# Performance work log

Hardware: AMD Instinct MI355X
Metric: run time of the kernel (lower is better)

The kernel has to match this reference:

```python
import jax, jax.numpy as jnp
import numpy as np

N = 100000; E = 1600000; G = 2000; S = 40; MAXP = 50
IN = 64; F = 128; H = 4; HD = F // H; FFN = 8 * F
EPS = 1e-5; BN_EPS = 1e-5

def _ln(x, g, b):
    m = jnp.mean(x, -1, keepdims=True)
    v = jnp.mean((x - m) ** 2, -1, keepdims=True)
    return (x - m) * jax.lax.rsqrt(v + EPS) * g + b

def setup_inputs():
    key = jax.random.key(0)
    ks = jax.random.split(key, 16)
    def lin(k, i, o):
        kw, kb = jax.random.split(k)
        lim = 1.0 / np.sqrt(i)
        return (jax.random.uniform(kw, (i, o), jnp.float32, -lim, lim),
                jax.random.uniform(kb, (o,), jnp.float32, -lim, lim))
    W_gcn, b_gcn = lin(ks[1], IN, F)
    Wq, bq = lin(ks[2], F, F); Wk, bk = lin(ks[3], F, F)
    Wv, bv = lin(ks[4], F, F); Wo, bo = lin(ks[5], F, F)
    W1, b1 = lin(ks[6], F, FFN); W2, b2 = lin(ks[7], FFN, F)
    Wg, bg = lin(ks[8], 2 * F, F)
    ones = lambda: jnp.ones((F,), jnp.float32)
    zeros = lambda: jnp.zeros((F,), jnp.float32)
    return {
        'x': jax.random.normal(ks[0], (N, IN), jnp.float32),
        'edge_index': jax.random.randint(ks[9], (2, E), 0, N),
        'batch': jnp.repeat(jnp.arange(G), N // G),
        'set_batch': jnp.repeat(jnp.arange(S), G // S),
        'W_gcn': W_gcn, 'b_gcn': b_gcn,
        'bn_g': ones(), 'bn_b': zeros(),
        'lnpre_g': ones(), 'lnpre_b': zeros(),
        'Wq': Wq, 'bq': bq, 'Wk': Wk, 'bk': bk, 'Wv': Wv, 'bv': bv, 'Wo': Wo, 'bo': bo,
        'ln1_g': ones(), 'ln1_b': zeros(),
        'W1': W1, 'b1': b1, 'W2': W2, 'b2': b2,
        'ln2_g': ones(), 'ln2_b': zeros(),
        'Wg': Wg, 'bg': bg,
    }

def _forward(x, W_gcn, b_gcn, bn_g, bn_b, lnpre_g, lnpre_b, Wq, bq, Wk, bk, Wv, bv, Wo, bo, ln1_g, ln1_b, W1, b1, W2, b2, ln2_g, ln2_b, Wg, bg, edge_index, batch, set_batch):
    row, col = edge_index[0], edge_index[1]
    # GCNConv, improved=True -> self-loop weight 2.0 (PyG gcn_norm)
    xw = x @ W_gcn                                              # [N,F]
    deg = jax.ops.segment_sum(jnp.ones(E, xw.dtype), col, N) + 2.0
    dinv = jax.lax.rsqrt(deg)
    norm = dinv[row] * dinv[col]                                # [E]
    agg = jax.ops.segment_sum(xw[row] * norm[:, None], col, N)  # scatter-add to targets
    h = agg + (2.0 * dinv * dinv)[:, None] * xw + b_gcn
    # BatchNorm1d eval (running_mean=0, running_var=1) + ReLU; dropout is identity in eval
    h = jax.nn.relu(h * jax.lax.rsqrt(jnp.asarray(1.0 + BN_EPS, h.dtype)) * bn_g + bn_b)
    # global mean pool per graph
    cnt_g = jax.ops.segment_sum(jnp.ones(N, h.dtype), batch, G)
    z = jax.ops.segment_sum(h, batch, G) / cnt_g[:, None]       # [G,F]
    # to_dense_batch over sets (set_batch is sorted)
    cnt_s = jax.ops.segment_sum(jnp.ones(G, jnp.int32), set_batch, S)
    starts = jnp.cumsum(cnt_s) - cnt_s
    pos = jnp.arange(G) - starts[set_batch]                     # position within set
    zd = jnp.zeros((S, MAXP, F), z.dtype).at[set_batch, pos].set(z)
    mask = jnp.arange(MAXP)[None, :] < cnt_s[:, None]           # [S,MAXP]
    # pre-LN MHA with key_padding_mask
    zn = _ln(zd, lnpre_g, lnpre_b)
    q = (zn @ Wq + bq).reshape(S, MAXP, H, HD)
    k = (zn @ Wk + bk).reshape(S, MAXP, H, HD)
    v = (zn @ Wv + bv).reshape(S, MAXP, H, HD)
    scores = jnp.einsum('sqhd,skhd->shqk', q, k) / np.sqrt(HD)
    scores = jnp.where(mask[:, None, None, :], scores, -1e9)
    attn = jax.nn.softmax(scores, -1)
    o = jnp.einsum('shqk,skhd->sqhd', attn, v).reshape(S, MAXP, F) @ Wo + bo
    zd = _ln(zd + o, ln1_g, ln1_b)
    # FFN block (post-LN residual)
    f = jax.nn.relu(zd @ W1 + b1) @ W2 + b2
    zd = _ln(zd + f, ln2_g, ln2_b)
    # z_dense[mask] ordering == gather via (set_batch, pos); broadcast to nodes
    set_info = zd[set_batch, pos][batch]                        # [N,F]
    # gated fusion
    gate = jax.nn.sigmoid(jnp.concatenate([h, set_info], -1) @ Wg + bg)
    return gate * set_info + (1.0 - gate) * h

def reference(x, edge_index, batch, set_batch, W_gcn, b_gcn, bn_g, bn_b, lnpre_g, lnpre_b, Wq, bq, Wk, bk, Wv, bv, Wo, bo, ln1_g, ln1_b, W1, b1, W2, b2, ln2_g, ln2_b, Wg, bg):
    return _forward(x, W_gcn, b_gcn, bn_g, bn_b, lnpre_g, lnpre_b, Wq, bq, Wk, bk, Wv, bv, Wo, bo, ln1_g, ln1_b, W1, b1, W2, b2, ln2_g, ln2_b, Wg, bg, edge_index, batch, set_batch)
```

## Files before the change

kernel.cpp:

```cpp
#include <hip/hip_runtime.h>
#include <hip/hip_bf16.h>
#include <cstddef>

#define NN 100000
#define NE 1600000
#define NG 2000
#define NS 40
#define INF 64
#define F 128
#define FFN_DIM 1024
#define NB 782
#define BCAP 3072
#define SC_BLOCKS 512
#define SC_CHUNK 3125
#define KSPLIT 8

using bf16 = __hip_bfloat16;
typedef __attribute__((ext_vector_type(8))) short short8;
typedef __attribute__((ext_vector_type(4))) float f32x4;
typedef __attribute__((ext_vector_type(2))) float f32x2;

__device__ __forceinline__ short f2bs(float f){
    union { bf16 b; short s; } u; u.b = __float2bfloat16(f); return u.s;
}
__device__ __forceinline__ unsigned int pk2(float a, float b){
    return (unsigned int)(unsigned short)f2bs(a) | ((unsigned int)(unsigned short)f2bs(b) << 16);
}

__global__ __launch_bounds__(256) void k_initw(int* __restrict__ bcursor,
                                               const float* __restrict__ Wq, const float* __restrict__ Wk,
                                               const float* __restrict__ Wv, const float* __restrict__ W1,
                                               const float* __restrict__ W2, const float* __restrict__ Wg,
                                               unsigned short* __restrict__ Wqb, unsigned short* __restrict__ Wkb,
                                               unsigned short* __restrict__ Wvb, unsigned short* __restrict__ W1b,
                                               unsigned short* __restrict__ W2b, unsigned short* __restrict__ Wgb){
    int t = blockIdx.x*256 + threadIdx.x;
    int stride = gridDim.x*256;
    for (int i=t; i<NB; i+=stride) bcursor[i] = i*BCAP;
    for (int i=t; i<16384; i+=stride){
        int k = i>>7, n = i&127;
        Wqb[n*128+k] = (unsigned short)f2bs(Wq[(size_t)k*F+n]);
        Wkb[n*128+k] = (unsigned short)f2bs(Wk[(size_t)k*F+n]);
        Wvb[n*128+k] = (unsigned short)f2bs(Wv[(size_t)k*F+n]);
        Wgb[n*128+k] = (unsigned short)f2bs(Wg[(size_t)k*F+n]);
    }
    for (int i=t; i<131072; i+=stride){
        int k = i>>10, n = i&1023;
        W1b[(size_t)n*128+k] = (unsigned short)f2bs(W1[(size_t)k*FFN_DIM+n]);
    }
    for (int i=t; i<131072; i+=stride){
        int n = i>>10, k = i&1023;
        W2b[(size_t)n*1024+k] = (unsigned short)f2bs(W2[(size_t)k*F+n]);
    }
}

__global__ __launch_bounds__(256) void k_xws(const float* __restrict__ x, const float* __restrict__ W,
                                             const float* __restrict__ dinv, unsigned char* __restrict__ xws8){
    __shared__ short Xs[128*72];
    __shared__ short Ws[128*72];
    int t = threadIdx.x;
    int rowBase = blockIdx.x * 128;
    #pragma unroll
    for (int i=0;i<32;i++){
        int id = i*256+t; int k = id>>7, n = id&127;
        Ws[n*72 + k] = f2bs(W[id]);
    }
    #pragma unroll
    for (int i=0;i<8;i++){
        int id = i*256+t;
        int r = id>>4; int k4 = (id&15)*4;
        int row = rowBase + r; if (row >= NN) row = NN-1;
        float4 v = *(const float4*)&x[(size_t)row*INF + k4];
        *(unsigned int*)&Xs[r*72 + k4]     = pk2(v.x, v.y);
        *(unsigned int*)&Xs[r*72 + k4 + 2] = pk2(v.z, v.w);
    }
// ... 10 lines not shown
        int kb = ks*32 + quad*8;
        short8 b0 = *(const short8*)&Xs[((w  )*16 + lr)*72 + kb];
        short8 b1 = *(const short8*)&Xs[((w+4)*16 + lr)*72 + kb];
        #pragma unroll
        for (int mt=0; mt<8; ++mt){
            short8 a = *(const short8*)&Ws[(mt*16 + lr)*72 + kb];
            acc[0][mt] = __builtin_amdgcn_mfma_f32_16x16x32_bf16(a, b0, acc[0][mt], 0, 0, 0);
            acc[1][mt] = __builtin_amdgcn_mfma_f32_16x16x32_bf16(a, b1, acc[1][mt], 0, 0, 0);
        }
    }
    #pragma unroll
    for (int rt=0; rt<2; ++rt){
        int row = rowBase + (w + rt*4)*16 + lr;
        if (row < NN){
            float dv = dinv[row];
            #pragma unroll
            for (int mt=0; mt<8; ++mt){
                int p = __builtin_amdgcn_cvt_pk_fp8_f32(acc[rt][mt][0]*dv, acc[rt][mt][1]*dv, 0, false);
                p     = __builtin_amdgcn_cvt_pk_fp8_f32(acc[rt][mt][2]*dv, acc[rt][mt][3]*dv, p, true);
                *(int*)&xws8[(size_t)row*F + mt*16 + quad*4] = p;
            }
        }
    }
}

__global__ __launch_bounds__(1024) void k_scatter2(const int* __restrict__ ei, int* __restrict__ bcursor,
                                                   int* __restrict__ ebuf){
    __shared__ int lh[NB];
    __shared__ int lb[NB];
    int t = threadIdx.x;
    int base = blockIdx.x * SC_CHUNK;
    for (int b=t; b<NB; b+=1024) lh[b] = 0;
    __syncthreads();
    int rr[4], cc[4];
    #pragma unroll
    for (int q=0;q<4;q++){
        int i = t + q*1024;
        bool v = (i < SC_CHUNK);
        int idx = v ? (base + i) : base;
        rr[q] = ei[idx];
        cc[q] = ei[NE + idx];
        if (v) atomicAdd(&lh[cc[q]>>7], 1);
    }
    __syncthreads();
    for (int b=t; b<NB; b+=1024){
        int n = lh[b];
        lb[b] = n ? atomicAdd(&bcursor[b], n) : 0;
        lh[b] = 0;
    }
    __syncthreads();
    #pragma unroll
    for (int q=0;q<4;q++){
        int i = t + q*1024;
        if (i < SC_CHUNK){
            int b = cc[q] >> 7;
            int rk = atomicAdd(&lh[b], 1);
            ebuf[lb[b] + rk] = (rr[q] << 7) | (cc[q] & 127);
        }
    }
}

__global__ __launch_bounds__(256) void k_sort(const int* __restrict__ ebuf, const int* __restrict__ bcursor,
                                              int* __restrict__ cnt, float* __restrict__ dinv,
                                              int* __restrict__ nstart, int* __restrict__ ebuf2){
    __shared__ int lh[128];
    __shared__ int s[128];
    __shared__ int lcur[128];
    __shared__ int sorted[BCAP];
    int t = threadIdx.x;
    int b = blockIdx.x;
    int e0 = b * BCAP;
    int nE = bcursor[b] - e0;
    if (t < 128) lh[t] = 0;
    __syncthreads();
    for (int i=t; i<nE; i+=256) atomicAdd(&lh[ebuf[e0+i] & 127], 1);
    __syncthreads();
    int c = (t < 128) ? lh[t] : 0;
    if (t < 128) s[t] = c;
    __syncthreads();
    #pragma unroll
    for (int off=1; off<128; off<<=1){
        int v = (t >= off && t < 128) ? s[t-off] : 0;
        __syncthreads();
        if (t < 128) s[t] += v;
        __syncthreads();
    }
    int node = b*128 + t;
    if (t < 128){
        int excl = s[t] - c;
        lcur[t] = excl;
        if (node < NN){
            nstart[node] = e0 + excl;
            cnt[node] = c;
            dinv[node] = rsqrtf((float)c + 2.0f);
        }
    }
    __syncthreads();
    for (int i=t; i<nE; i+=256){
        int v = ebuf[e0 + i];
        int nl = v & 127;
        int rk = atomicAdd(&lcur[nl], 1);
        sorted[rk] = (v >> 7) << 5;
    }
    __syncthreads();
    for (int i=t; i<nE; i+=256) ebuf2[e0 + i] = sorted[i];
}

__global__ __launch_bounds__(256) void k_aggpool(const unsigned char* __restrict__ xws8,
                                                 const int* __restrict__ nstart, const int* __restrict__ cnt,
                                                 const float* __restrict__ dinv, const float* __restrict__ b_gcn,
                                                 const float* __restrict__ bn_g, const float* __restrict__ bn_b,
                                                 const int* __restrict__ ebuf2,
                                                 const float* __restrict__ lnpre_g, const float* __restrict__ lnpre_b,
                                                 float* __restrict__ h, unsigned short* __restrict__ hb,
                                                 float* __restrict__ z, unsigned short* __restrict__ znb){
    __shared__ float zacc[4][128];
    int t = threadIdx.x;
    int lane = t & 63, w = t >> 6;
    int half = lane >> 5, lh = lane & 31;
    int g = blockIdx.x;
    const unsigned int* xw32 = (const unsigned int*)xws8;
    unsigned int* hb32 = (unsigned int*)hb;
    unsigned int* znb32 = (unsigned int*)znb;

    float4 bg4  = *(const float4*)&b_gcn[4*lh];
    float4 bng4 = *(const float4*)&bn_g[4*lh];
    float4 bnb4 = *(const float4*)&bn_b[4*lh];
    const float bns = rsqrtf(1.f + 1e-5f);
// ... 75 lines not shown
        float s2 = ((v0.z+v1.z)+(v2.z+v3.z)) / 50.0f;
        float s3 = ((v0.w+v1.w)+(v2.w+v3.w)) / 50.0f;
        if (half == 0)
            *(float4*)&z[(size_t)g*F + 4*lh] = make_float4(s0,s1,s2,s3);
        float s = (s0+s1)+(s2+s3);
        #pragma unroll
        for (int off=1; off<32; off<<=1) s += __shfl_xor(s, off);
        float m = s * (1.f/128.f);
        float d0=s0-m, d1=s1-m, d2=s2-m, d3=s3-m;
        float vv = (d0*d0+d1*d1)+(d2*d2+d3*d3);
        #pragma unroll
        for (int off=1; off<32; off<<=1) vv += __shfl_xor(vv, off);
        float rs = rsqrtf(vv*(1.f/128.f) + 1e-5f);
        float4 lg = *(const float4*)&lnpre_g[4*lh];
        float4 lb = *(const float4*)&lnpre_b[4*lh];
        if (half == 0){
            float o0 = d0*rs*lg.x+lb.x, o1 = d1*rs*lg.y+lb.y;
            float o2 = d2*rs*lg.z+lb.z, o3 = d3*rs*lg.w+lb.w;
            *(uint2*)&znb32[(size_t)g*64 + 2*lh] = make_uint2(pk2(o0,o1), pk2(o2,o3));
        }
    }
}

__global__ __launch_bounds__(256) void k_qkv_g(const unsigned short* __restrict__ znb,
                                               const unsigned short* __restrict__ Wqb,
                                               const unsigned short* __restrict__ Wkb,
                                               const unsigned short* __restrict__ Wvb,
                                               const float* __restrict__ bq, const float* __restrict__ bk,
                                               const float* __restrict__ bv,
                                               float* __restrict__ Cq, float* __restrict__ Ck,
                                               float* __restrict__ Cv){
    int zsel = blockIdx.z;
    const unsigned short* B = (zsel==0)?Wqb:(zsel==1)?Wkb:Wvb;
    const float* bias = (zsel==0)?bq:(zsel==1)?bk:bv;
    float* C = (zsel==0)?Cq:(zsel==1)?Ck:Cv;
    int t = threadIdx.x;
    int lane = t & 63, w = t >> 6;
    int lr = lane & 15, quad = lane >> 4;
    int mrow0 = blockIdx.x*64 + w*16;
    f32x4 acc[8];
    #pragma unroll
    for (int j=0;j<8;j++) acc[j] = (f32x4){0.f,0.f,0.f,0.f};
    #pragma unroll
    for (int ks=0; ks<4; ++ks){
        int kb = ks*32 + quad*8;
        int row = mrow0 + lr;
        if (row >= NG) row = NG-1;
        short8 a = *(const short8*)&znb[(size_t)row*F + kb];
        #pragma unroll
        for (int nt=0; nt<8; ++nt){
            short8 b = *(const short8*)&B[(size_t)(nt*16 + lr)*128 + kb];
            acc[nt] = __builtin_amdgcn_mfma_f32_16x16x32_bf16(a, b, acc[nt], 0, 0, 0);
        }
    }
    #pragma unroll
    for (int r=0; r<4; ++r){
        int row = mrow0 + quad*4 + r;
        if (row >= NG) continue;
        #pragma unroll
        for (int nt=0; nt<8; ++nt){
            int col = nt*16 + lr;
            C[(size_t)row*F + col] = acc[nt][r] + bias[col];
        }
    }
}

__global__ __launch_bounds__(256) void k_ffn1_g(const unsigned short* __restrict__ zd1b,
                                                const unsigned short* __restrict__ W1b,
                                                const float* __restrict__ b1,
                                                unsigned short* __restrict__ ffn1b){
    int t = threadIdx.x;
    int lane = t & 63, w = t >> 6;
    int lr = lane & 15, quad = lane >> 4;
    int mrow0 = blockIdx.x*64 + w*16;
    int colBase = blockIdx.y*128;
    f32x4 acc[8];
    #pragma unroll
    for (int j=0;j<8;j++) acc[j] = (f32x4){0.f,0.f,0.f,0.f};
    #pragma unroll
    for (int ks=0; ks<4; ++ks){
        int kb = ks*32 + quad*8;
        int row = mrow0 + lr;
        if (row >= NG) row = NG-1;
        short8 a = *(const short8*)&zd1b[(size_t)row*F + kb];
        #pragma unroll
        for (int nt=0; nt<8; ++nt){
            short8 b = *(const short8*)&W1b[(size_t)(colBase + nt*16 + lr)*128 + kb];
            acc[nt] = __builtin_amdgcn_mfma_f32_16x16x32_bf16(a, b, acc[nt], 0, 0, 0);
        }
    }
    #pragma unroll
    for (int r=0; r<4; ++r){
        int row = mrow0 + quad*4 + r;
        if (row >= NG) continue;
        #pragma unroll
        for (int nt=0; nt<8; ++nt){
            int col = colBase + nt*16 + lr;
            ffn1b[(size_t)row*FFN_DIM + col] = (unsigned short)f2bs(fmaxf(acc[nt][r] + b1[col], 0.f));
        }
    }
}

__global__ __launch_bounds__(256) void k_ffn2_g(const unsigned short* __restrict__ ffn1b,
                                                const unsigned short* __restrict__ W2b,
                                                float* __restrict__ part){
    int t = threadIdx.x;
    int lane = t & 63, w = t >> 6;
    int lr = lane & 15, quad = lane >> 4;
    int mrow0 = blockIdx.x*64 + w*16;
    int kbeg = blockIdx.z*128;
    f32x4 acc[8];
    #pragma unroll
    for (int j=0;j<8;j++) acc[j] = (f32x4){0.f,0.f,0.f,0.f};
    #pragma unroll
    for (int ks=0; ks<4; ++ks){
        int kb = ks*32 + quad*8;
        int row = mrow0 + lr;
        if (row >= NG) row = NG-1;
        short8 a = *(const short8*)&ffn1b[(size_t)row*FFN_DIM + kbeg + kb];
        #pragma unroll
        for (int nt=0; nt<8; ++nt){
            short8 b = *(const short8*)&W2b[(size_t)(nt*16 + lr)*1024 + kbeg + kb];
            acc[nt] = __builtin_amdgcn_mfma_f32_16x16x32_bf16(a, b, acc[nt], 0, 0, 0);
        }
    }
    float* Cp = part + (size_t)blockIdx.z*NG*F;
    #pragma unroll
    for (int r=0; r<4; ++r){
        int row = mrow0 + quad*4 + r;
        if (row >= NG) continue;
        #pragma unroll
        for (int nt=0; nt<8; ++nt){
            int col = nt*16 + lr;
            Cp[(size_t)row*F + col] = acc[nt][r];
        }
    }
}

__global__ __launch_bounds__(256) void k_wo_ln(const float* __restrict__ ao, const float* __restrict__ Wo,
                                               const float* __restrict__ bo, const float* __restrict__ z,
                                               const float* __restrict__ g, const float* __restrict__ b,
                                               float* __restrict__ zd1, unsigned short* __restrict__ zd1b){
    __shared__ float As[32*36];
    __shared__ float Bs[32*128];
    int t = threadIdx.x;
    int rowBase = blockIdx.x*32;
    int c0 = (t&31)*4, r0 = (t>>5)*4;
    unsigned int* zd1b32 = (unsigned int*)zd1b;
    float acc[4][4];
    #pragma unroll
    for (int i=0;i<4;i++){ acc[i][0]=0.f; acc[i][1]=0.f; acc[i][2]=0.f; acc[i][3]=0.f; }
    for (int kb=0; kb<F; kb+=32){
        #pragma unroll
        for (int i=0;i<4;i++){
            int id = i*256+t; int kk = id&31; int r = id>>5;
            int row = rowBase + r;
            As[kk*36+r] = (row<NG) ? ao[(size_t)row*F + kb + kk] : 0.f;
        }
        #pragma unroll
        for (int i=0;i<16;i++){
            int id = i*256+t; int c = id&127; int kk = id>>7;
            Bs[kk*128+c] = Wo[(size_t)(kb+kk)*F + c];
        }
        __syncthreads();
        for (int kk=0;kk<32;kk++){
            float4 a = *(const float4*)&As[kk*36+r0];
            float4 bv = *(const float4*)&Bs[kk*128+c0];
            float av[4]={a.x,a.y,a.z,a.w}; float bb[4]={bv.x,bv.y,bv.z,bv.w};
            #pragma unroll
            for(int i=0;i<4;i++)
                #pragma unroll
                for(int j=0;j<4;j++) acc[i][j] += av[i]*bb[j];
        }
        __syncthreads();
    }
    float4 bo4 = *(const float4*)&bo[c0];
    float4 g4  = *(const float4*)&g[c0];
    float4 b4  = *(const float4*)&b[c0];
    #pragma unroll
    for (int i=0;i<4;i++){
        int row = rowBase + r0 + i;
        float v0=0.f,v1=0.f,v2=0.f,v3=0.f;
        if (row < NG){
            float4 zr = *(const float4*)&z[(size_t)row*F + c0];
            v0 = acc[i][0] + bo4.x + zr.x;
            v1 = acc[i][1] + bo4.y + zr.y;
            v2 = acc[i][2] + bo4.z + zr.z;
            v3 = acc[i][3] + bo4.w + zr.w;
        }
        float s = (v0+v1)+(v2+v3);
        #pragma unroll
        for (int off=1; off<32; off<<=1) s += __shfl_xor(s, off);
        float m = s * (1.f/128.f);
        float d0=v0-m, d1=v1-m, d2=v2-m, d3=v3-m;
        float vv = (d0*d0+d1*d1)+(d2*d2+d3*d3);
        #pragma unroll
        for (int off=1; off<32; off<<=1) vv += __shfl_xor(vv, off);
        float rs = rsqrtf(vv*(1.f/128.f) + 1e-5f);
        if (row < NG){
            float o0 = d0*rs*g4.x+b4.x, o1 = d1*rs*g4.y+b4.y;
            float o2 = d2*rs*g4.z+b4.z, o3 = d3*rs*g4.w+b4.w;
            *(float4*)&zd1[(size_t)row*F + c0] = make_float4(o0,o1,o2,o3);
            *(uint2*)&zd1b32[(size_t)row*(F/2) + c0/2] = make_uint2(pk2(o0,o1), pk2(o2,o3));
        }
    }
}

__global__ __launch_bounds__(256) void k_ln_red_gsi(const float* __restrict__ A, const float* __restrict__ part,
                                                    const float* __restrict__ bias, const float* __restrict__ g,
                                                    const float* __restrict__ b, const float* __restrict__ Wb,
                                                    const float* __restrict__ bg, float* __restrict__ zd2,
                                                    float* __restrict__ gsi){
    __shared__ float Zs[4][128];
    __shared__ float Bs[32*128];
    int t = threadIdx.x; int lane = t&63;
    int rquad = t>>6;
    int row = blockIdx.x*4 + rquad;
    int i0 = row*F + 2*lane;
    float x0 = A[i0] + bias[2*lane], x1 = A[i0+1] + bias[2*lane+1];
    #pragma unroll
    for (int zz=0; zz<KSPLIT; ++zz){
        x0 += part[(size_t)zz*NG*F + i0];
        x1 += part[(size_t)zz*NG*F + i0 + 1];
    }
    float s = x0+x1;
    for (int off=1; off<64; off<<=1) s += __shfl_xor(s, off);
    float m = s * (1.f/128.f);
    float d0 = x0-m, d1 = x1-m;
    float vv = d0*d0 + d1*d1;
    for (int off=1; off<64; off<<=1) vv += __shfl_xor(vv, off);
    float rs = rsqrtf(vv*(1.f/128.f) + 1e-5f);
    float o0 = d0*rs*g[2*lane]   + b[2*lane];
    float o1 = d1*rs*g[2*lane+1] + b[2*lane+1];
    zd2[i0]   = o0;
    zd2[i0+1] = o1;
    Zs[rquad][2*lane]   = o0;
    Zs[rquad][2*lane+1] = o1;
    __syncthreads();
    int col = t & 127, rp = t >> 7;
    float a0=0.f, a1=0.f;
    for (int kb=0; kb<F; kb+=32){
        #pragma unroll
        for (int i=0;i<16;i++){
            int id = i*256+t; int c = id&127; int kk = id>>7;
            Bs[kk*128+c] = Wb[(size_t)(kb+kk)*F + c];
        }
        __syncthreads();
        for (int kk=0;kk<32;kk++){
            float w = Bs[kk*128+col];
            a0 += Zs[rp][kb+kk]   * w;
            a1 += Zs[rp+2][kb+kk] * w;
        }
        __syncthreads();
    }
    float bgc = bg[col];
    gsi[(size_t)(blockIdx.x*4 + rp)*F + col]     = a0 + bgc;
    gsi[(size_t)(blockIdx.x*4 + rp + 2)*F + col] = a1 + bgc;
}

__global__ __launch_bounds__(256) void k_attn(const float* __restrict__ q, const float* __restrict__ k,
                                              const float* __restrict__ v, float* __restrict__ o){
    __shared__ float Qs[1600], Ks[1600], Vs[1600], Sc[2500];
    int t = threadIdx.x;
    int s = blockIdx.x >> 2; int hh = blockIdx.x & 3;
    for (int idx=t; idx<1600; idx+=256){
        int i = idx>>5, d = idx&31;
        size_t gi = (size_t)(s*50+i)*F + hh*32 + d;
        Qs[idx]=q[gi]; Ks[idx]=k[gi]; Vs[idx]=v[gi];
    }
    __syncthreads();
    for (int idx=t; idx<2500; idx+=256){
        int qi = idx/50, ki = idx%50;
        float acc=0.f;
        #pragma unroll 8
        for (int d=0;d<32;d++) acc += Qs[qi*32+d]*Ks[ki*32+d];
        Sc[idx] = acc * 0.17677669529663687f;
    }
    __syncthreads();
    if (t < 50){
        float m=-1e30f;
        for (int j=0;j<50;j++) m = fmaxf(m, Sc[t*50+j]);
        float sum=0.f;
        for (int j=0;j<50;j++){ float e=__expf(Sc[t*50+j]-m); Sc[t*50+j]=e; sum+=e; }
        float inv = 1.f/sum;
        for (int j=0;j<50;j++) Sc[t*50+j] *= inv;
    }
    __syncthreads();
    for (int idx=t; idx<1600; idx+=256){
        int qi = idx>>5, d = idx&31;
        float acc=0.f;
        #pragma unroll 10
        for (int ki=0;ki<50;ki++) acc += Sc[qi*50+ki]*Vs[ki*32+d];
        o[(size_t)(s*50+qi)*F + hh*32 + d] = acc;
    }
}

__global__ __launch_bounds__(256) void k_gate_mfma(const float* __restrict__ h,
                                                   const unsigned short* __restrict__ hb,
                                                   const unsigned short* __restrict__ Wgb,
                                                   const float* __restrict__ gsi, const float* __restrict__ zd2,
                                                   float* __restrict__ out){
    int t = threadIdx.x;
    int lane = t & 63, w = t >> 6;
    int lr = lane & 15, quad = lane >> 4;
    int mrow0 = blockIdx.x*64 + w*16;
    f32x4 acc[8];
    #pragma unroll
    for (int j=0;j<8;j++) acc[j] = (f32x4){0.f,0.f,0.f,0.f};
    #pragma unroll
    for (int ks=0; ks<4; ++ks){
        int kb = ks*32 + quad*8;
        int row = mrow0 + lr;
        if (row >= NN) row = NN-1;
        short8 a = *(const short8*)&hb[(size_t)row*F + kb];
        #pragma unroll
        for (int nt=0; nt<8; ++nt){
// ... 60 lines not shown
    int*   nstart= (int*)(ws + o);   o += (size_t)NN*4;
    int*   ebuf  = (int*)(ws + o);   o += (size_t)NB*BCAP*4;
    int*   ebuf2 = (int*)(ws + o);   o += (size_t)NB*BCAP*4;
    float* dinv  = (float*)(ws + o); o += (size_t)NN*4;
    int*   bcursor=(int*)(ws + o);   o += 1024*4;
    unsigned short* Wgb = (unsigned short*)(ws + o); o += 16384*2;
    unsigned short* Wqb = (unsigned short*)(ws + o); o += 16384*2;
    unsigned short* Wkb = (unsigned short*)(ws + o); o += 16384*2;
    unsigned short* Wvb = (unsigned short*)(ws + o); o += 16384*2;
    unsigned short* W1b = (unsigned short*)(ws + o); o += (size_t)131072*2;
    unsigned short* W2b = (unsigned short*)(ws + o); o += (size_t)131072*2;
    float* z     = (float*)(ws + o); o += (size_t)NG*F*4;
    unsigned short* znb = (unsigned short*)(ws + o); o += (size_t)NG*F*2;
    float* qb    = (float*)(ws + o); o += (size_t)NG*F*4;
    float* kb2   = (float*)(ws + o); o += (size_t)NG*F*4;
    float* vb    = (float*)(ws + o); o += (size_t)NG*F*4;
    float* ao    = (float*)(ws + o); o += (size_t)NG*F*4;
    float* zd1   = (float*)(ws + o); o += (size_t)NG*F*4;
    unsigned short* zd1b = (unsigned short*)(ws + o); o += (size_t)NG*F*2;
    unsigned short* ffn1b = (unsigned short*)(ws + o); o += (size_t)NG*FFN_DIM*2;
    float* part  = (float*)(ws + o); o += (size_t)KSPLIT*NG*F*4;
    float* zd2   = (float*)(ws + o); o += (size_t)NG*F*4;
    float* gsi   = (float*)(ws + o); o += (size_t)NG*F*4;

    k_initw<<<64, 256, 0, stream>>>(bcursor, Wq, Wk, Wv, W1, W2, Wg,
                                    Wqb, Wkb, Wvb, W1b, W2b, Wgb);
    k_scatter2<<<SC_BLOCKS, 1024, 0, stream>>>(ei, bcursor, ebuf);
    k_sort<<<NB, 256, 0, stream>>>(ebuf, bcursor, cnt, dinv, nstart, ebuf2);
    k_xws<<<(NN+127)/128, 256, 0, stream>>>(x, W_gcn, dinv, xws8);
    k_aggpool<<<NG, 256, 0, stream>>>(xws8, nstart, cnt, dinv, b_gcn, bn_g, bn_b, ebuf2,
                                      lnpre_g, lnpre_b, h, hb, z, znb);

    dim3 gqkv((NG+63)/64, 1, 3);
    k_qkv_g<<<gqkv, 256, 0, stream>>>(znb, Wqb, Wkb, Wvb, bq, bk, bv, qb, kb2, vb);
    k_attn<<<NS*4, 256, 0, stream>>>(qb, kb2, vb, ao);
    k_wo_ln<<<(NG+31)/32, 256, 0, stream>>>(ao, Wo, bo, z, ln1_g, ln1_b, zd1, zd1b);
    dim3 gffn1((NG+63)/64, FFN_DIM/128);
    k_ffn1_g<<<gffn1, 256, 0, stream>>>(zd1b, W1b, b1, ffn1b);
    dim3 gffn2((NG+63)/64, 1, KSPLIT);
    k_ffn2_g<<<gffn2, 256, 0, stream>>>(ffn1b, W2b, part);
    k_ln_red_gsi<<<NG/4, 256, 0, stream>>>(zd1, part, b2, ln2_g, ln2_b,
                                           Wg + (size_t)F*F, bg, zd2, gsi);

    k_gate_mfma<<<(NN+63)/64, 256, 0, stream>>>(h, hb, Wgb, gsi, zd2, out);
}
```

Baseline: 330.8 us.

## Merge front-end and transformer chain kernels into cooperative persistent kernels

Replaces the weight-init, edge-scatter and bucket-sort launches with one cooperative kernel that separates phases with grid.sync. It likewise folds the QKV, attention, Wo+LN, FFN1, FFN2 and LN+gate-input launches into a single 256-block cooperative kernel. The aim is to remove per-launch overhead and inter-kernel gaps in the small-work transformer stages. In exchange, the fixed 256-block grid lowers parallelism for the scatter and sort phases, and each grid.sync carries its own cost.

```diff
diff --git a/kernel.cpp b/kernel.cpp
--- a/kernel.cpp
+++ b/kernel.cpp
@@ -1,6 +1,9 @@
 #include <hip/hip_runtime.h>
 #include <hip/hip_bf16.h>
+#include <hip/hip_cooperative_groups.h>
 #include <cstddef>
+
+namespace cg = cooperative_groups;
 
 #define NN 100000
 #define NE 1600000
@@ -27,30 +30,115 @@
     return (unsigned int)(unsigned short)f2bs(a) | ((unsigned int)(unsigned short)f2bs(b) << 16);
 }
 
-__global__ __launch_bounds__(256) void k_initw(int* __restrict__ bcursor,
-                                               const float* __restrict__ Wq, const float* __restrict__ Wk,
-                                               const float* __restrict__ Wv, const float* __restrict__ W1,
-                                               const float* __restrict__ W2, const float* __restrict__ Wg,
-                                               unsigned short* __restrict__ Wqb, unsigned short* __restrict__ Wkb,
-                                               unsigned short* __restrict__ Wvb, unsigned short* __restrict__ W1b,
-                                               unsigned short* __restrict__ W2b, unsigned short* __restrict__ Wgb){
-    int t = blockIdx.x*256 + threadIdx.x;
-    int stride = gridDim.x*256;
-    for (int i=t; i<NB; i+=stride) bcursor[i] = i*BCAP;
-    for (int i=t; i<16384; i+=stride){
+__global__ __launch_bounds__(1024) void k_front(int* __restrict__ bcursor, const int* __restrict__ ei,
+                                                int* __restrict__ ebuf, int* __restrict__ cnt,
+                                                float* __restrict__ dinv, int* __restrict__ nstart,
+                                                int* __restrict__ ebuf2,
+                                                const float* __restrict__ Wq, const float* __restrict__ Wk,
+                                                const float* __restrict__ Wv, const float* __restrict__ W1,
+                                                const float* __restrict__ W2, const float* __restrict__ Wg,
+                                                unsigned short* __restrict__ Wqb, unsigned short* __restrict__ Wkb,
+                                                unsigned short* __restrict__ Wvb, unsigned short* __restrict__ W1b,
+                                                unsigned short* __restrict__ W2b, unsigned short* __restrict__ Wgb){
+    cg::grid_group grid = cg::this_grid();
+    __shared__ int lh[NB];
+    __shared__ int lb[NB];
+    __shared__ int s_s[128];
+    __shared__ int s_lcur[128];
+    __shared__ int sorted[BCAP];
+    int t = threadIdx.x;
+    int gt = blockIdx.x*1024 + t;
+    int gstride = gridDim.x*1024;
+
+    for (int i=gt; i<NB; i+=gstride) bcursor[i] = i*BCAP;
+    for (int i=gt; i<16384; i+=gstride){
         int k = i>>7, n = i&127;
         Wqb[n*128+k] = (unsigned short)f2bs(Wq[(size_t)k*F+n]);
         Wkb[n*128+k] = (unsigned short)f2bs(Wk[(size_t)k*F+n]);
         Wvb[n*128+k] = (unsigned short)f2bs(Wv[(size_t)k*F+n]);
         Wgb[n*128+k] = (unsigned short)f2bs(Wg[(size_t)k*F+n]);
     }
-    for (int i=t; i<131072; i+=stride){
+    for (int i=gt; i<131072; i+=gstride){
         int k = i>>10, n = i&1023;
         W1b[(size_t)n*128+k] = (unsigned short)f2bs(W1[(size_t)k*FFN_DIM+n]);
     }
-    for (int i=t; i<131072; i+=stride){
+    for (int i=gt; i<131072; i+=gstride){
         int n = i>>10, k = i&1023;
         W2b[(size_t)n*1024+k] = (unsigned short)f2bs(W2[(size_t)k*F+n]);
+    }
+    grid.sync();
+
+    for (int chunk = blockIdx.x; chunk < SC_BLOCKS; chunk += gridDim.x){
+        int base = chunk * SC_CHUNK;
+        for (int b=t; b<NB; b+=1024) lh[b] = 0;
+        __syncthreads();
+        int rr[4], cc[4];
+        #pragma unroll
+        for (int q=0;q<4;q++){
+            int i = t + q*1024;
+            bool v = (i < SC_CHUNK);
+            int idx = v ? (base + i) : base;
+            rr[q] = ei[idx];
+            cc[q] = ei[NE + idx];
+            if (v) atomicAdd(&lh[cc[q]>>7], 1);
+        }
+        __syncthreads();
+        for (int b=t; b<NB; b+=1024){
+            int n = lh[b];
+            lb[b] = n ? atomicAdd(&bcursor[b], n) : 0;
+            lh[b] = 0;
+        }
+        __syncthreads();
+        #pragma unroll
+        for (int q=0;q<4;q++){
+            int i = t + q*1024;
+            if (i < SC_CHUNK){
+                int b = cc[q] >> 7;
+                int rk = atomicAdd(&lh[b], 1);
+                ebuf[lb[b] + rk] = (rr[q] << 7) | (cc[q] & 127);
+            }
+        }
+        __syncthreads();
+    }
+    grid.sync();
+
+    for (int b = blockIdx.x; b < NB; b += gridDim.x){
+        int e0 = b * BCAP;
+        int nE = bcursor[b] - e0;
+        if (t < 128) lh[t] = 0;
+        __syncthreads();
+        for (int i=t; i<nE; i+=1024) atomicAdd(&lh[ebuf[e0+i] & 127], 1);
+        __syncthreads();
+        int c = (t < 128) ? lh[t] : 0;
+        if (t < 128) s_s[t] = c;
+        __syncthreads();
+        #pragma unroll
+        for (int off=1; off<128; off<<=1){
+            int v = (t >= off && t < 128) ? s_s[t-off] : 0;
+            __syncthreads();
+            if (t < 128) s_s[t] += v;
+            __syncthreads();
+        }
+        int node = b*128 + t;
+        if (t < 128){
+            int excl = s_s[t] - c;
+            s_lcur[t] = excl;
+            if (node < NN){
+                nstart[node] = e0 + excl;
+                cnt[node] = c;
+                dinv[node] = rsqrtf((float)c + 2.0f);
+            }
+        }
+        __syncthreads();
+        for (int i=t; i<nE; i+=1024){
+            int v = ebuf[e0 + i];
+            int nl = v & 127;
+            int rk = atomicAdd(&s_lcur[nl], 1);
+            sorted[rk] = (v >> 7) << 5;
+        }
+        __syncthreads();
+        for (int i=t; i<nE; i+=1024) ebuf2[e0 + i] = sorted[i];
+        __syncthreads();
     }
 }
 
@@ -107,88 +195,6 @@
             }
         }
     }
-}
-
-__global__ __launch_bounds__(1024) void k_scatter2(const int* __restrict__ ei, int* __restrict__ bcursor,
-                                                   int* __restrict__ ebuf){
-    __shared__ int lh[NB];
-    __shared__ int lb[NB];
-    int t = threadIdx.x;
-    int base = blockIdx.x * SC_CHUNK;
-    for (int b=t; b<NB; b+=1024) lh[b] = 0;
-    __syncthreads();
-    int rr[4], cc[4];
-    #pragma unroll
-    for (int q=0;q<4;q++){
-        int i = t + q*1024;
-        bool v = (i < SC_CHUNK);
-        int idx = v ? (base + i) : base;
-        rr[q] = ei[idx];
-        cc[q] = ei[NE + idx];
-        if (v) atomicAdd(&lh[cc[q]>>7], 1);
-    }
-    __syncthreads();
-    for (int b=t; b<NB; b+=1024){
-        int n = lh[b];
-        lb[b] = n ? atomicAdd(&bcursor[b], n) : 0;
-        lh[b] = 0;
-    }
-    __syncthreads();
-    #pragma unroll
-    for (int q=0;q<4;q++){
-        int i = t + q*1024;
-        if (i < SC_CHUNK){
-            int b = cc[q] >> 7;
-            int rk = atomicAdd(&lh[b], 1);
-            ebuf[lb[b] + rk] = (rr[q] << 7) | (cc[q] & 127);
-        }
-    }
-}
-
-__global__ __launch_bounds__(256) void k_sort(const int* __restrict__ ebuf, const int* __restrict__ bcursor,
-                                              int* __restrict__ cnt, float* __restrict__ dinv,
-                                              int* __restrict__ nstart, int* __restrict__ ebuf2){
-    __shared__ int lh[128];
-    __shared__ int s[128];
-    __shared__ int lcur[128];
-    __shared__ int sorted[BCAP];
-    int t = threadIdx.x;
-    int b = blockIdx.x;
-    int e0 = b * BCAP;
-    int nE = bcursor[b] - e0;
-    if (t < 128) lh[t] = 0;
-    __syncthreads();
-    for (int i=t; i<nE; i+=256) atomicAdd(&lh[ebuf[e0+i] & 127], 1);
-    __syncthreads();
-    int c = (t < 128) ? lh[t] : 0;
-    if (t < 128) s[t] = c;
-    __syncthreads();
-    #pragma unroll
-    for (int off=1; off<128; off<<=1){
-        int v = (t >= off && t < 128) ? s[t-off] : 0;
-        __syncthreads();
-        if (t < 128) s[t] += v;
-        __syncthreads();
-    }
-    int node = b*128 + t;
-    if (t < 128){
-        int excl = s[t] - c;
-        lcur[t] = excl;
-        if (node < NN){
-            nstart[node] = e0 + excl;
-            cnt[node] = c;
-            dinv[node] = rsqrtf((float)c + 2.0f);
-        }
-    }
-    __syncthreads();
-    for (int i=t; i<nE; i+=256){
-        int v = ebuf[e0 + i];
-        int nl = v & 127;
-        int rk = atomicAdd(&lcur[nl], 1);
-        sorted[rk] = (v >> 7) << 5;
-    }
-    __syncthreads();
-    for (int i=t; i<nE; i+=256) ebuf2[e0 + i] = sorted[i];
 }
 
 __global__ __launch_bounds__(256) void k_aggpool(const unsigned char* __restrict__ xws8,
@@ -310,276 +316,283 @@
     }
 }
 
-__global__ __launch_bounds__(256) void k_qkv_g(const unsigned short* __restrict__ znb,
+__global__ __launch_bounds__(256) void k_chain(const unsigned short* __restrict__ znb,
+                                               const float* __restrict__ z,
                                                const unsigned short* __restrict__ Wqb,
                                                const unsigned short* __restrict__ Wkb,
                                                const unsigned short* __restrict__ Wvb,
                                                const float* __restrict__ bq, const float* __restrict__ bk,
                                                const float* __restrict__ bv,
-                                               float* __restrict__ Cq, float* __restrict__ Ck,
-                                               float* __restrict__ Cv){
-    int zsel = blockIdx.z;
-    const unsigned short* B = (zsel==0)?Wqb:(zsel==1)?Wkb:Wvb;
-    const float* bias = (zsel==0)?bq:(zsel==1)?bk:bv;
-    float* C = (zsel==0)?Cq:(zsel==1)?Ck:Cv;
+                                               float* __restrict__ qb, float* __restrict__ kb2,
+                                               float* __restrict__ vb, float* __restrict__ ao,
+                                               const float* __restrict__ Wo, const float* __restrict__ bo,
+                                               const float* __restrict__ ln1_g, const float* __restrict__ ln1_b,
+                                               float* __restrict__ zd1, unsigned short* __restrict__ zd1b,
+                                               const unsigned short* __restrict__ W1b, const float* __restrict__ b1,
+                                               unsigned short* __restrict__ ffn1b,
+                                               const unsigned short* __restrict__ W2b, float* __restrict__ part,
+                                               const float* __restrict__ b2, const float* __restrict__ ln2_g,
+                                               const float* __restrict__ ln2_b, const float* __restrict__ Wgbot,
+                                               const float* __restrict__ bg, float* __restrict__ zd2,
+                                               float* __restrict__ gsi){
+    cg::grid_group grid = cg::this_grid();
+    __shared__ __align__(16) char cs[29248];
     int t = threadIdx.x;
     int lane = t & 63, w = t >> 6;
     int lr = lane & 15, quad = lane >> 4;
-    int mrow0 = blockIdx.x*64 + w*16;
-    f32x4 acc[8];
-    #pragma unroll
-    for (int j=0;j<8;j++) acc[j] = (f32x4){0.f,0.f,0.f,0.f};
-    #pragma unroll
-    for (int ks=0; ks<4; ++ks){
-        int kb = ks*32 + quad*8;
-        int row = mrow0 + lr;
-        if (row >= NG) row = NG-1;
-        short8 a = *(const short8*)&znb[(size_t)row*F + kb];
-        #pragma unroll
-        for (int nt=0; nt<8; ++nt){
-            short8 b = *(const short8*)&B[(size_t)(nt*16 + lr)*128 + kb];
-            acc[nt] = __builtin_amdgcn_mfma_f32_16x16x32_bf16(a, b, acc[nt], 0, 0, 0);
-        }
-    }
-    #pragma unroll
-    for (int r=0; r<4; ++r){
-        int row = mrow0 + quad*4 + r;
-        if (row >= NG) continue;
-        #pragma unroll
-        for (int nt=0; nt<8; ++nt){
-            int col = nt*16 + lr;
-            C[(size_t)row*F + col] = acc[nt][r] + bias[col];
-        }
-    }
-}
-
-__global__ __launch_bounds__(256) void k_ffn1_g(const unsigned short* __restrict__ zd1b,
-                                                const unsigned short* __restrict__ W1b,
-                                                const float* __restrict__ b1,
-                                                unsigned short* __restrict__ ffn1b){
-    int t = threadIdx.x;
-    int lane = t & 63, w = t >> 6;
-    int lr = lane & 15, quad = lane >> 4;
-    int mrow0 = blockIdx.x*64 + w*16;
-    int colBase = blockIdx.y*128;
-    f32x4 acc[8];
-    #pragma unroll
-    for (int j=0;j<8;j++) acc[j] = (f32x4){0.f,0.f,0.f,0.f};
-    #pragma unroll
-    for (int ks=0; ks<4; ++ks){
-        int kb = ks*32 + quad*8;
-        int row = mrow0 + lr;
-        if (row >= NG) row = NG-1;
-        short8 a = *(const short8*)&zd1b[(size_t)row*F + kb];
-        #pragma unroll
-        for (int nt=0; nt<8; ++nt){
-            short8 b = *(const short8*)&W1b[(size_t)(colBase + nt*16 + lr)*128 + kb];
-            acc[nt] = __builtin_amdgcn_mfma_f32_16x16x32_bf16(a, b, acc[nt], 0, 0, 0);
-        }
-    }
-    #pragma unroll
-    for (int r=0; r<4; ++r){
-        int row = mrow0 + quad*4 + r;
-        if (row >= NG) continue;
-        #pragma unroll
-        for (int nt=0; nt<8; ++nt){
-            int col = colBase + nt*16 + lr;
-            ffn1b[(size_t)row*FFN_DIM + col] = (unsigned short)f2bs(fmaxf(acc[nt][r] + b1[col], 0.f));
-        }
-    }
-}
-
-__global__ __launch_bounds__(256) void k_ffn2_g(const unsigned short* __restrict__ ffn1b,
-                                                const unsigned short* __restrict__ W2b,
-                                                float* __restrict__ part){
-    int t = threadIdx.x;
-    int lane = t & 63, w = t >> 6;
-    int lr = lane & 15, quad = lane >> 4;
-    int mrow0 = blockIdx.x*64 + w*16;
-    int kbeg = blockIdx.z*128;
-    f32x4 acc[8];
-    #pragma unroll
-    for (int j=0;j<8;j++) acc[j] = (f32x4){0.f,0.f,0.f,0.f};
-    #pragma unroll
-    for (int ks=0; ks<4; ++ks){
-        int kb = ks*32 + quad*8;
-        int row = mrow0 + lr;
-        if (row >= NG) row = NG-1;
-        short8 a = *(const short8*)&ffn1b[(size_t)row*FFN_DIM + kbeg + kb];
-        #pragma unroll
-        for (int nt=0; nt<8; ++nt){
-            short8 b = *(const short8*)&W2b[(size_t)(nt*16 + lr)*1024 + kbeg + kb];
-            acc[nt] = __builtin_amdgcn_mfma_f32_16x16x32_bf16(a, b, acc[nt], 0, 0, 0);
-        }
-    }
-    float* Cp = part + (size_t)blockIdx.z*NG*F;
-    #pragma unroll
-    for (int r=0; r<4; ++r){
-        int row = mrow0 + quad*4 + r;
-        if (row >= NG) continue;
-        #pragma unroll
-        for (int nt=0; nt<8; ++nt){
-            int col = nt*16 + lr;
-            Cp[(size_t)row*F + col] = acc[nt][r];
-        }
-    }
-}
-
-__global__ __launch_bounds__(256) void k_wo_ln(const float* __restrict__ ao, const float* __restrict__ Wo,
-                                               const float* __restrict__ bo, const float* __restrict__ z,
-                                               const float* __restrict__ g, const float* __restrict__ b,
-                                               float* __restrict__ zd1, unsigned short* __restrict__ zd1b){
-    __shared__ float As[32*36];
-    __shared__ float Bs[32*128];
-    int t = threadIdx.x;
-    int rowBase = blockIdx.x*32;
-    int c0 = (t&31)*4, r0 = (t>>5)*4;
     unsigned int* zd1b32 = (unsigned int*)zd1b;
-    float acc[4][4];
-    #pragma unroll
-    for (int i=0;i<4;i++){ acc[i][0]=0.f; acc[i][1]=0.f; acc[i][2]=0.f; acc[i][3]=0.f; }
-    for (int kb=0; kb<F; kb+=32){
+
+    for (int u = blockIdx.x; u < 96; u += gridDim.x){
+        int zsel = u >> 5, rt = u & 31;
+        const unsigned short* B = (zsel==0)?Wqb:(zsel==1)?Wkb:Wvb;
+        const float* bias = (zsel==0)?bq:(zsel==1)?bk:bv;
+        float* C = (zsel==0)?qb:(zsel==1)?kb2:vb;
+        int mrow0 = rt*64 + w*16;
+        f32x4 acc[8];
+        #pragma unroll
+        for (int j=0;j<8;j++) acc[j] = (f32x4){0.f,0.f,0.f,0.f};
+        #pragma unroll
+        for (int ks=0; ks<4; ++ks){
+            int kb = ks*32 + quad*8;
+            int row = mrow0 + lr;
+            if (row >= NG) row = NG-1;
+            short8 a = *(const short8*)&znb[(size_t)row*F + kb];
+            #pragma unroll
+            for (int nt=0; nt<8; ++nt){
+                short8 b = *(const short8*)&B[(size_t)(nt*16 + lr)*128 + kb];
+                acc[nt] = __builtin_amdgcn_mfma_f32_16x16x32_bf16(a, b, acc[nt], 0, 0, 0);
+            }
+        }
+        #pragma unroll
+        for (int r=0; r<4; ++r){
+            int row = mrow0 + quad*4 + r;
+            if (row >= NG) continue;
+            #pragma unroll
+            for (int nt=0; nt<8; ++nt){
+                int col = nt*16 + lr;
+                C[(size_t)row*F + col] = acc[nt][r] + bias[col];
+            }
+        }
+    }
+    grid.sync();
+
+    for (int u = blockIdx.x; u < NS*4; u += gridDim.x){
+        float* Qs = (float*)cs;
+        float* Ks = (float*)(cs + 6400);
+        float* Vs = (float*)(cs + 12800);
+        float* Sc = (float*)(cs + 19200);
+        int s = u >> 2; int hh = u & 3;
+        for (int idx=t; idx<1600; idx+=256){
+            int i = idx>>5, d = idx&31;
+            size_t gi = (size_t)(s*50+i)*F + hh*32 + d;
+            Qs[idx]=qb[gi]; Ks[idx]=kb2[gi]; Vs[idx]=vb[gi];
+        }
+        __syncthreads();
+        for (int idx=t; idx<2500; idx+=256){
+            int qi = idx/50, ki = idx%50;
+            float acc=0.f;
+            #pragma unroll 8
+            for (int d=0;d<32;d++) acc += Qs[qi*32+d]*Ks[ki*32+d];
+            Sc[idx] = acc * 0.17677669529663687f;
+        }
+        __syncthreads();
+        if (t < 50){
+            float m=-1e30f;
+            for (int j=0;j<50;j++) m = fmaxf(m, Sc[t*50+j]);
+            float sum=0.f;
+            for (int j=0;j<50;j++){ float e=__expf(Sc[t*50+j]-m); Sc[t*50+j]=e; sum+=e; }
+            float inv = 1.f/sum;
+            for (int j=0;j<50;j++) Sc[t*50+j] *= inv;
+        }
+        __syncthreads();
+        for (int idx=t; idx<1600; idx+=256){
+            int qi = idx>>5, d = idx&31;
+            float acc=0.f;
+            #pragma unroll 10
+            for (int ki=0;ki<50;ki++) acc += Sc[qi*50+ki]*Vs[ki*32+d];
+            ao[(size_t)(s*50+qi)*F + hh*32 + d] = acc;
+        }
+        __syncthreads();
+    }
+    grid.sync();
+
+    for (int u = blockIdx.x; u < 63; u += gridDim.x){
+        float* As = (float*)cs;
+        float* Bs = (float*)(cs + 4608);
+        int rowBase = u*32;
+        int c0 = (t&31)*4, r0 = (t>>5)*4;
+        float acc[4][4];
+        #pragma unroll
+        for (int i=0;i<4;i++){ acc[i][0]=0.f; acc[i][1]=0.f; acc[i][2]=0.f; acc[i][3]=0.f; }
+        for (int kb=0; kb<F; kb+=32){
+            #pragma unroll
+            for (int i=0;i<4;i++){
+                int id = i*256+t; int kk = id&31; int r = id>>5;
+                int row = rowBase + r;
+                As[kk*36+r] = (row<NG) ? ao[(size_t)row*F + kb + kk] : 0.f;
+            }
+            #pragma unroll
+            for (int i=0;i<16;i++){
+                int id = i*256+t; int c = id&127; int kk = id>>7;
+                Bs[kk*128+c] = Wo[(size_t)(kb+kk)*F + c];
+            }
+            __syncthreads();
+            for (int kk=0;kk<32;kk++){
+                float4 a = *(const float4*)&As[kk*36+r0];
+                float4 bv4 = *(const float4*)&Bs[kk*128+c0];
+                float av[4]={a.x,a.y,a.z,a.w}; float bb[4]={bv4.x,bv4.y,bv4.z,bv4.w};
+                #pragma unroll
+                for(int i=0;i<4;i++)
+                    #pragma unroll
+                    for(int j=0;j<4;j++) acc[i][j] += av[i]*bb[j];
+            }
+            __syncthreads();
+        }
+        float4 bo4 = *(const float4*)&bo[c0];
+        float4 g4  = *(const float4*)&ln1_g[c0];
+        float4 b4  = *(const float4*)&ln1_b[c0];
         #pragma unroll
         for (int i=0;i<4;i++){
-            int id = i*256+t; int kk = id&31; int r = id>>5;
-            int row = rowBase + r;
-            As[kk*36+r] = (row<NG) ? ao[(size_t)row*F + kb + kk] : 0.f;
-        }
-        #pragma unroll
-        for (int i=0;i<16;i++){
-            int id = i*256+t; int c = id&127; int kk = id>>7;
-            Bs[kk*128+c] = Wo[(size_t)(kb+kk)*F + c];
-        }
-        __syncthreads();
-        for (int kk=0;kk<32;kk++){
-            float4 a = *(const float4*)&As[kk*36+r0];
-            float4 bv = *(const float4*)&Bs[kk*128+c0];
-            float av[4]={a.x,a.y,a.z,a.w}; float bb[4]={bv.x,bv.y,bv.z,bv.w};
-            #pragma unroll
-            for(int i=0;i<4;i++)
-                #pragma unroll
-                for(int j=0;j<4;j++) acc[i][j] += av[i]*bb[j];
-        }
-        __syncthreads();
-    }
-    float4 bo4 = *(const float4*)&bo[c0];
-    float4 g4  = *(const float4*)&g[c0];
-    float4 b4  = *(const float4*)&b[c0];
-    #pragma unroll
-    for (int i=0;i<4;i++){
-        int row = rowBase + r0 + i;
-        float v0=0.f,v1=0.f,v2=0.f,v3=0.f;
-        if (row < NG){
-            float4 zr = *(const float4*)&z[(size_t)row*F + c0];
-            v0 = acc[i][0] + bo4.x + zr.x;
-            v1 = acc[i][1] + bo4.y + zr.y;
-            v2 = acc[i][2] + bo4.z + zr.z;
-            v3 = acc[i][3] + bo4.w + zr.w;
-        }
-        float s = (v0+v1)+(v2+v3);
-        #pragma unroll
-        for (int off=1; off<32; off<<=1) s += __shfl_xor(s, off);
+            int row = rowBase + r0 + i;
+            float v0=0.f,v1=0.f,v2=0.f,v3=0.f;
+            if (row < NG){
+                float4 zr = *(const float4*)&z[(size_t)row*F + c0];
+                v0 = acc[i][0] + bo4.x + zr.x;
+                v1 = acc[i][1] + bo4.y + zr.y;
+                v2 = acc[i][2] + bo4.z + zr.z;
+                v3 = acc[i][3] + bo4.w + zr.w;
+            }
+            float s = (v0+v1)+(v2+v3);
+            #pragma unroll
+            for (int off=1; off<32; off<<=1) s += __shfl_xor(s, off);
+            float m = s * (1.f/128.f);
+            float d0=v0-m, d1=v1-m, d2=v2-m, d3=v3-m;
+            float vv = (d0*d0+d1*d1)+(d2*d2+d3*d3);
+            #pragma unroll
+            for (int off=1; off<32; off<<=1) vv += __shfl_xor(vv, off);
+            float rs = rsqrtf(vv*(1.f/128.f) + 1e-5f);
+            if (row < NG){
+                float o0 = d0*rs*g4.x+b4.x, o1 = d1*rs*g4.y+b4.y;
+                float o2 = d2*rs*g4.z+b4.z, o3 = d3*rs*g4.w+b4.w;
+                *(float4*)&zd1[(size_t)row*F + c0] = make_float4(o0,o1,o2,o3);
+                *(uint2*)&zd1b32[(size_t)row*(F/2) + c0/2] = make_uint2(pk2(o0,o1), pk2(o2,o3));
+            }
+        }
+        __syncthreads();
+    }
+    grid.sync();
+
+    for (int u = blockIdx.x; u < 256; u += gridDim.x){
+        int rt = u & 31, ct = u >> 5;
+        int mrow0 = rt*64 + w*16;
+        int colBase = ct*128;
+        f32x4 acc[8];
+        #pragma unroll
+        for (int j=0;j<8;j++) acc[j] = (f32x4){0.f,0.f,0.f,0.f};
+        #pragma unroll
+        for (int ks=0; ks<4; ++ks){
+            int kb = ks*32 + quad*8;
+            int row = mrow0 + lr;
+            if (row >= NG) row = NG-1;
+            short8 a = *(const short8*)&zd1b[(size_t)row*F + kb];
+            #pragma unroll
+            for (int nt=0; nt<8; ++nt){
+                short8 b = *(const short8*)&W1b[(size_t)(colBase + nt*16 + lr)*128 + kb];
+                acc[nt] = __builtin_amdgcn_mfma_f32_16x16x32_bf16(a, b, acc[nt], 0, 0, 0);
+            }
+        }
+        #pragma unroll
+        for (int r=0; r<4; ++r){
+            int row = mrow0 + quad*4 + r;
+            if (row >= NG) continue;
+            #pragma unroll
+            for (int nt=0; nt<8; ++nt){
+                int col = colBase + nt*16 + lr;
+                ffn1b[(size_t)row*FFN_DIM + col] = (unsigned short)f2bs(fmaxf(acc[nt][r] + b1[col], 0.f));
+            }
+        }
+    }
+    grid.sync();
+
+    for (int u = blockIdx.x; u < 256; u += gridDim.x){
+        int rt = u & 31, kc = u >> 5;
+        int mrow0 = rt*64 + w*16;
+        int kbeg = kc*128;
+        f32x4 acc[8];
+        #pragma unroll
+        for (int j=0;j<8;j++) acc[j] = (f32x4){0.f,0.f,0.f,0.f};
+        #pragma unroll
+        for (int ks=0; ks<4; ++ks){
+            int kb = ks*32 + quad*8;
+            int row = mrow0 + lr;
+            if (row >= NG) row = NG-1;
+            short8 a = *(const short8*)&ffn1b[(size_t)row*FFN_DIM + kbeg + kb];
+            #pragma unroll
+            for (int nt=0; nt<8; ++nt){
+                short8 b = *(const short8*)&W2b[(size_t)(nt*16 + lr)*1024 + kbeg + kb];
+                acc[nt] = __builtin_amdgcn_mfma_f32_16x16x32_bf16(a, b, acc[nt], 0, 0, 0);
+            }
+        }
+        float* Cp = part + (size_t)kc*NG*F;
+        #pragma unroll
+        for (int r=0; r<4; ++r){
+            int row = mrow0 + quad*4 + r;
+            if (row >= NG) continue;
+            #pragma unroll
+            for (int nt=0; nt<8; ++nt){
+                int col = nt*16 + lr;
+                Cp[(size_t)row*F + col] = acc[nt][r];
+            }
+        }
+    }
+    grid.sync();
+
+    for (int u = blockIdx.x; u < NG/4; u += gridDim.x){
+        float* Zs = (float*)cs;
+        float* Bs = (float*)(cs + 2048);
+        int rquad = t>>6;
+        int row = u*4 + rquad;
+        int i0 = row*F + 2*lane;
+        float x0 = zd1[i0] + b2[2*lane], x1 = zd1[i0+1] + b2[2*lane+1];
+        #pragma unroll
+        for (int zz=0; zz<KSPLIT; ++zz){
+            x0 += part[(size_t)zz*NG*F + i0];
+            x1 += part[(size_t)zz*NG*F + i0 + 1];
+        }
+        float s = x0+x1;
+        for (int off=1; off<64; off<<=1) s += __shfl_xor(s, off);
         float m = s * (1.f/128.f);
-        float d0=v0-m, d1=v1-m, d2=v2-m, d3=v3-m;
-        float vv = (d0*d0+d1*d1)+(d2*d2+d3*d3);
-        #pragma unroll
-        for (int off=1; off<32; off<<=1) vv += __shfl_xor(vv, off);
+        float d0 = x0-m, d1 = x1-m;
+        float vv = d0*d0 + d1*d1;
+        for (int off=1; off<64; off<<=1) vv += __shfl_xor(vv, off);
         float rs = rsqrtf(vv*(1.f/128.f) + 1e-5f);
-        if (row < NG){
-            float o0 = d0*rs*g4.x+b4.x, o1 = d1*rs*g4.y+b4.y;
-            float o2 = d2*rs*g4.z+b4.z, o3 = d3*rs*g4.w+b4.w;
-            *(float4*)&zd1[(size_t)row*F + c0] = make_float4(o0,o1,o2,o3);
-            *(uint2*)&zd1b32[(size_t)row*(F/2) + c0/2] = make_uint2(pk2(o0,o1), pk2(o2,o3));
-        }
-    }
-}
-
-__global__ __launch_bounds__(256) void k_ln_red_gsi(const float* __restrict__ A, const float* __restrict__ part,
-                                                    const float* __restrict__ bias, const float* __restrict__ g,
-                                                    const float* __restrict__ b, const float* __restrict__ Wb,
-                                                    const float* __restrict__ bg, float* __restrict__ zd2,
-                                                    float* __restrict__ gsi){
-    __shared__ float Zs[4][128];
-    __shared__ float Bs[32*128];
-    int t = threadIdx.x; int lane = t&63;
-    int rquad = t>>6;
-    int row = blockIdx.x*4 + rquad;
-    int i0 = row*F + 2*lane;
-    float x0 = A[i0] + bias[2*lane], x1 = A[i0+1] + bias[2*lane+1];
-    #pragma unroll
-    for (int zz=0; zz<KSPLIT; ++zz){
-        x0 += part[(size_t)zz*NG*F + i0];
-        x1 += part[(size_t)zz*NG*F + i0 + 1];
-    }
-    float s = x0+x1;
-    for (int off=1; off<64; off<<=1) s += __shfl_xor(s, off);
-    float m = s * (1.f/128.f);
-    float d0 = x0-m, d1 = x1-m;
-    float vv = d0*d0 + d1*d1;
-    for (int off=1; off<64; off<<=1) vv += __shfl_xor(vv, off);
-    float rs = rsqrtf(vv*(1.f/128.f) + 1e-5f);
-    float o0 = d0*rs*g[2*lane]   + b[2*lane];
-    float o1 = d1*rs*g[2*lane+1] + b[2*lane+1];
-    zd2[i0]   = o0;
-    zd2[i0+1] = o1;
-    Zs[rquad][2*lane]   = o0;
-    Zs[rquad][2*lane+1] = o1;
-    __syncthreads();
-    int col = t & 127, rp = t >> 7;
-    float a0=0.f, a1=0.f;
-    for (int kb=0; kb<F; kb+=32){
-        #pragma unroll
-        for (int i=0;i<16;i++){
-            int id = i*256+t; int c = id&127; int kk = id>>7;
-            Bs[kk*128+c] = Wb[(size_t)(kb+kk)*F + c];
-        }
-        __syncthreads();
-        for (int kk=0;kk<32;kk++){
-            float w = Bs[kk*128+col];
-            a0 += Zs[rp][kb+kk]   * w;
-            a1 += Zs[rp+2][kb+kk] * w;
-        }
-        __syncthreads();
-    }
-    float bgc = bg[col];
-    gsi[(size_t)(blockIdx.x*4 + rp)*F + col]     = a0 + bgc;
-    gsi[(size_t)(blockIdx.x*4 + rp + 2)*F + col] = a1 + bgc;
-}
-
-__global__ __launch_bounds__(256) void k_attn(const float* __restrict__ q, const float* __restrict__ k,
-                                              const float* __restrict__ v, float* __restrict__ o){
-    __shared__ float Qs[1600], Ks[1600], Vs[1600], Sc[2500];
-    int t = threadIdx.x;
-    int s = blockIdx.x >> 2; int hh = blockIdx.x & 3;
-    for (int idx=t; idx<1600; idx+=256){
-        int i = idx>>5, d = idx&31;
-        size_t gi = (size_t)(s*50+i)*F + hh*32 + d;
-        Qs[idx]=q[gi]; Ks[idx]=k[gi]; Vs[idx]=v[gi];
-    }
-    __syncthreads();
-    for (int idx=t; idx<2500; idx+=256){
-        int qi = idx/50, ki = idx%50;
-        float acc=0.f;
-        #pragma unroll 8
-        for (int d=0;d<32;d++) acc += Qs[qi*32+d]*Ks[ki*32+d];
-        Sc[idx] = acc * 0.17677669529663687f;
-    }
-    __syncthreads();
-    if (t < 50){
-        float m=-1e30f;
-        for (int j=0;j<50;j++) m = fmaxf(m, Sc[t*50+j]);
-        float sum=0.f;
-        for (int j=0;j<50;j++){ float e=__expf(Sc[t*50+j]-m); Sc[t*50+j]=e; sum+=e; }
-        float inv = 1.f/sum;
-        for (int j=0;j<50;j++) Sc[t*50+j] *= inv;
-    }
-    __syncthreads();
-    for (int idx=t; idx<1600; idx+=256){
-        int qi = idx>>5, d = idx&31;
-        float acc=0.f;
-        #pragma unroll 10
-        for (int ki=0;ki<50;ki++) acc += Sc[qi*50+ki]*Vs[ki*32+d];
-        o[(size_t)(s*50+qi)*F + hh*32 + d] = acc;
+        float o0 = d0*rs*ln2_g[2*lane]   + ln2_b[2*lane];
+        float o1 = d1*rs*ln2_g[2*lane+1] + ln2_b[2*lane+1];
+        zd2[i0]   = o0;
+        zd2[i0+1] = o1;
+        Zs[rquad*128 + 2*lane]   = o0;
+        Zs[rquad*128 + 2*lane+1] = o1;
+        __syncthreads();
+        int col = t & 127, rp = t >> 7;
+        float a0=0.f, a1=0.f;
+        for (int kb=0; kb<F; kb+=32){
+            #pragma unroll
+            for (int i=0;i<16;i++){
+                int id = i*256+t; int c = id&127; int kk = id>>7;
+                Bs[kk*128+c] = Wgbot[(size_t)(kb+kk)*F + c];
+            }
+            __syncthreads();
+            for (int kk=0;kk<32;kk++){
+                float wv = Bs[kk*128+col];
+                a0 += Zs[rp*128 + kb+kk]     * wv;
+                a1 += Zs[(rp+2)*128 + kb+kk] * wv;
+            }
+            __syncthreads();
+        }
+        float bgc = bg[col];
+        gsi[(size_t)(u*4 + rp)*F + col]     = a0 + bgc;
+        gsi[(size_t)(u*4 + rp + 2)*F + col] = a1 + bgc;
+        __syncthreads();
     }
 }
 
@@ -686,25 +699,29 @@
     float* part  = (float*)(ws + o); o += (size_t)KSPLIT*NG*F*4;
     float* zd2   = (float*)(ws + o); o += (size_t)NG*F*4;
     float* gsi   = (float*)(ws + o); o += (size_t)NG*F*4;
-
-    k_initw<<<64, 256, 0, stream>>>(bcursor, Wq, Wk, Wv, W1, W2, Wg,
-                                    Wqb, Wkb, Wvb, W1b, W2b, Wgb);
-    k_scatter2<<<SC_BLOCKS, 1024, 0, stream>>>(ei, bcursor, ebuf);
-    k_sort<<<NB, 256, 0, stream>>>(ebuf, bcursor, cnt, dinv, nstart, ebuf2);
+    const float* Wgbot = Wg + (size_t)F*F;
+
+    {
+        void* fargs[] = { (void*)&bcursor, (void*)&ei, (void*)&ebuf, (void*)&cnt, (void*)&dinv,
+                          (void*)&nstart, (void*)&ebuf2,
+                          (void*)&Wq, (void*)&Wk, (void*)&Wv, (void*)&W1, (void*)&W2, (void*)&Wg,
+                          (void*)&Wqb, (void*)&Wkb, (void*)&Wvb, (void*)&W1b, (void*)&W2b, (void*)&Wgb };
+        hipLaunchCooperativeKernel((const void*)k_front, dim3(256), dim3(1024), fargs, 0, stream);
+    }
     k_xws<<<(NN+127)/128, 256, 0, stream>>>(x, W_gcn, dinv, xws8);
     k_aggpool<<<NG, 256, 0, stream>>>(xws8, nstart, cnt, dinv, b_gcn, bn_g, bn_b, ebuf2,
                                       lnpre_g, lnpre_b, h, hb, z, znb);
 
-    dim3 gqkv((NG+63)/64, 1, 3);
-    k_qkv_g<<<gqkv, 256, 0, stream>>>(znb, Wqb, Wkb, Wvb, bq, bk, bv, qb, kb2, vb);
-    k_attn<<<NS*4, 256, 0, stream>>>(qb, kb2, vb, ao);
-    k_wo_ln<<<(NG+31)/32, 256, 0, stream>>>(ao, Wo, bo, z, ln1_g, ln1_b, zd1, zd1b);
-    dim3 gffn1((NG+63)/64, FFN_DIM/128);
-    k_ffn1_g<<<gffn1, 256, 0, stream>>>(zd1b, W1b, b1, ffn1b);
-    dim3 gffn2((NG+63)/64, 1, KSPLIT);
-    k_ffn2_g<<<gffn2, 256, 0, stream>>>(ffn1b, W2b, part);
-    k_ln_red_gsi<<<NG/4, 256, 0, stream>>>(zd1, part, b2, ln2_g, ln2_b,
-                                           Wg + (size_t)F*F, bg, zd2, gsi);
+    {
+        void* cargs[] = { (void*)&znb, (void*)&z, (void*)&Wqb, (void*)&Wkb, (void*)&Wvb,
+                          (void*)&bq, (void*)&bk, (void*)&bv,
+                          (void*)&qb, (void*)&kb2, (void*)&vb, (void*)&ao,
+                          (void*)&Wo, (void*)&bo, (void*)&ln1_g, (void*)&ln1_b,
+                          (void*)&zd1, (void*)&zd1b, (void*)&W1b, (void*)&b1, (void*)&ffn1b,
+                          (void*)&W2b, (void*)&part, (void*)&b2, (void*)&ln2_g, (void*)&ln2_b,
+                          (void*)&Wgbot, (void*)&bg, (void*)&zd2, (void*)&gsi };
+        hipLaunchCooperativeKernel((const void*)k_chain, dim3(256), dim3(256), cargs, 0, stream);
+    }
 
     k_gate_mfma<<<(NN+63)/64, 256, 0, stream>>>(h, hb, Wgb, gsi, zd2, out);
 }
```

After: 579.7 us. 1.75x slower.
